# Optimization experiments

Measured on AMD Instinct MI355X. Metric: run time of the kernel, lower is better.

Reference implementation:

```python
import jax, jax.numpy as jnp
import numpy as np

N_ATOMS = 16384
N_EDGES = 524288
N_MOL = 256
A = 4            # num_pseudo_species
S = 4            # len(unique_numbers)
NMAX = 10        # radial basis size
NSPH = 9         # (l_max+1)^2 with l_max=2
Q = A * NMAX
NL = 3           # l_max+1
F = Q * Q * NL   # 4800 power-spectrum features
CUTOFF = 5.0
AVG_ATOMS = 64.0
SCALE = 1.0
H1, H2 = 512, 512


def _sph_l012(u):
    # real spherical harmonics l=0,1,2 on unit vectors u [E,3] -> [E,9]
    x, y, z = u[:, 0], u[:, 1], u[:, 2]
    c1 = 0.4886025119029199
    c2 = 1.0925484305920792
    return jnp.stack([
        jnp.full_like(x, 0.28209479177387814),
        c1 * y, c1 * z, c1 * x,
        c2 * x * y, c2 * y * z,
        0.31539156525252005 * (3.0 * z * z - 1.0),
        c2 * x * z,
        0.5462742152960396 * (x * x - y * y),
    ], axis=-1)


def _forward(positions, cells, edge_offsets, U, gamma, beta, W1, W2, W3, Wc,
             numbers, edge_indices, batch):
    send, recv = edge_indices[0], edge_indices[1]
    cell_e = cells[batch[send]]                                  # [E,3,3]
    rvec = positions[recv] - positions[send] + jnp.einsum('ek,ekl->el', edge_offsets, cell_e)
    r = jnp.sqrt(jnp.sum(rvec * rvec, axis=-1) + 1e-12)          # [E]
    rhat = rvec / r[:, None]
    fc = 0.5 * (jnp.cos(jnp.pi * r / CUTOFF) + 1.0) * (r < CUTOFF)
    mu = jnp.linspace(0.0, CUTOFF, NMAX)
    sig = CUTOFF / NMAX
    R = jnp.exp(-((r[:, None] - mu) ** 2) / (2.0 * sig * sig)) * fc[:, None]  # [E,NMAX]
    Y = _sph_l012(rhat)                                          # [E,9]
    RY = jnp.einsum('en,ek->enk', R, Y)                          # [E,NMAX,9]
    w = U[:, numbers[send]]                                      # [A,E] pseudo-species mix of neighbor species
    # spherical expansion per atom: c[i,a,n,lm]
    c = jnp.stack([jax.ops.segment_sum(w[a][:, None, None] * RY, recv, num_segments=N_ATOMS)
                   for a in range(A)], axis=1)                   # [N,A,NMAX,9]
    c = c.reshape(N_ATOMS, Q, NSPH)
    # power spectrum: contract over m within each l block, normalize by sqrt(2l+1)
    lblocks = [(0, 1, 1.0), (1, 4, 3.0), (4, 9, 5.0)]
    ps = jnp.stack([jnp.einsum('iqm,ipm->iqp', c[:, :, a:b], c[:, :, a:b]) / jnp.sqrt(nl)
                    for a, b, nl in lblocks], axis=-1).reshape(N_ATOMS, F)
    # layer norm
    mean = ps.mean(axis=-1, keepdims=True)
    var = ps.var(axis=-1, keepdims=True)
    x = (ps - mean) / jnp.sqrt(var + 1e-5) * gamma + beta

    def contract(x, W):
        # species-indexed contraction: per-species weight via combination matrix U
        Wsp = jnp.einsum('as,aio->sio', U, W)                    # [S,in,out]
        out = jnp.zeros((x.shape[0], W.shape[-1]), x.dtype)
        for s in range(S):                                       # small fixed species set
            out = out + jnp.where((numbers == s)[:, None], x @ Wsp[s], 0.0)
        return out

    x = jax.nn.silu(contract(x, W1))
    x = jax.nn.silu(contract(x, W2))
    x = contract(x, W3)                                          # [N,1]
    e = jax.ops.segment_sum(x, batch, num_segments=N_MOL)        # [M,1]
    e = e / jnp.sqrt(float(A)) / AVG_ATOMS
    comp = jax.ops.segment_sum(jax.nn.one_hot(numbers, S, dtype=x.dtype), batch, num_segments=N_MOL)
    return e * SCALE + comp @ Wc.T


def setup_inputs() -> dict:
    key = jax.random.key(0)
    ks = jax.random.split(key, 10)
    positions = jax.random.normal(ks[0], (N_ATOMS, 3), dtype=jnp.float32)
    cells = jnp.zeros((N_MOL, 3, 3), dtype=jnp.float32)
    numbers = jax.random.randint(ks[1], (N_ATOMS,), 0, S)
    edge_indices = jax.random.randint(ks[2], (2, N_EDGES), 0, N_ATOMS)
    edge_offsets = jnp.zeros((N_EDGES, 3), dtype=jnp.float32)
    batch = jnp.sort(jax.random.randint(ks[3], (N_ATOMS,), 0, N_MOL))
    U = jax.random.normal(ks[4], (A, S), dtype=jnp.float32) * 0.5
    gamma = jnp.ones((F,), dtype=jnp.float32)
    beta = jnp.zeros((F,), dtype=jnp.float32)
    W1 = jax.random.normal(ks[5], (A, F, H1), dtype=jnp.float32) / np.sqrt(F)
    W2 = jax.random.normal(ks[6], (A, H1, H2), dtype=jnp.float32) / np.sqrt(H1)
    W3 = jax.random.normal(ks[7], (A, H2, 1), dtype=jnp.float32) / np.sqrt(H2)
    Wc = jax.random.normal(ks[8], (1, S), dtype=jnp.float32) * 0.1
    return {"positions": positions, "cells": cells, "numbers": numbers,
            "edge_indices": edge_indices, "edge_offsets": edge_offsets, "batch": batch,
            "U": U, "gamma": gamma, "beta": beta, "W1": W1, "W2": W2, "W3": W3, "Wc": Wc}


def reference(positions, cells, numbers, edge_indices, edge_offsets, batch,
              U, gamma, beta, W1, W2, W3, Wc):
    return _forward(positions, cells, edge_offsets, U, gamma, beta, W1, W2, W3, Wc,
                    numbers, edge_indices, batch)
```

## Files before the change

kernel.cpp:

```cpp
#include <hip/hip_runtime.h>

#define NA   16384
#define NE   524288
#define NM   256
#define FF   4800
#define FR   2688
#define HH   512
#define NMX  10
#define NSPH 9

typedef __bf16 bf16x8 __attribute__((ext_vector_type(8)));
typedef float  f32x4  __attribute__((ext_vector_type(4)));
typedef unsigned short u16x8 __attribute__((ext_vector_type(8)));

__device__ inline unsigned short f2bf(float x){
  unsigned int u = __builtin_bit_cast(unsigned int, x);
  u += 0x7fffu + ((u >> 16) & 1u);
  return (unsigned short)(u >> 16);
}
__device__ inline float bf2f(unsigned short h){
  unsigned int u = ((unsigned int)h) << 16;
  return __builtin_bit_cast(float, u);
}
__device__ inline void atomic_add_f(float* p, float v){
  __hip_atomic_fetch_add(p, v, __ATOMIC_RELAXED, __HIP_MEMORY_SCOPE_AGENT);
}
__device__ inline void gload16(const void* g, void* l){
  __builtin_amdgcn_global_load_lds(
      (const __attribute__((address_space(1))) unsigned int*)g,
      (__attribute__((address_space(3))) unsigned int*)l, 16, 0, 0);
}
__device__ inline float silu(float x){ return x / (1.f + __expf(-x)); }

__device__ inline void decode_blk(int b, int& qb, int& pb){
  int q = 0, rem = b;
  while (rem >= 10 - q){ rem -= 10 - q; q++; }
  qb = q; pb = q + rem;
}

template<int CNT>
__device__ inline void ps_block(const float* __restrict__ cl, int qb, int pb, int off,
                                float nrm, bool diag, unsigned short* ob,
                                float& s1, float& s2){
  float cq[4][CNT], cp[4][CNT];
  #pragma unroll
  for (int i = 0; i < 4; i++)
    #pragma unroll
    for (int k = 0; k < CNT; k++){
      cq[i][k] = cl[(qb*4 + i)*9 + off + k];
      cp[i][k] = cl[(pb*4 + i)*9 + off + k];
    }
  #pragma unroll
  for (int qi = 0; qi < 4; qi++)
    #pragma unroll
    for (int pi = 0; pi < 4; pi++){
      float v = 0.f;
      #pragma unroll
      for (int k = 0; k < CNT; k++) v += cq[qi][k] * cp[pi][k];
      v *= nrm;
      float wgt = diag ? ((qi < pi) ? 2.f : ((qi == pi) ? 1.f : 0.f)) : 2.f;
      if (diag && qi > pi) v = 0.f;
      ob[qi*4 + pi] = f2bf(v);
      s1 += wgt * v;
      s2 += wgt * v * v;
    }
}

template<int CNT>
__device__ inline void ps_block_half(const float* __restrict__ cl, int qb, int pb, int off,
                                     float nrm, bool diag, int qh, unsigned short* ob,
                                     float& s1, float& s2){
  float cq[2][CNT], cp[4][CNT];
  #pragma unroll
  for (int i = 0; i < 2; i++)
    #pragma unroll
    for (int k = 0; k < CNT; k++)
      cq[i][k] = cl[(qb*4 + qh*2 + i)*9 + off + k];
  #pragma unroll
  for (int i = 0; i < 4; i++)
    #pragma unroll
    for (int k = 0; k < CNT; k++)
      cp[i][k] = cl[(pb*4 + i)*9 + off + k];
  #pragma unroll
  for (int qi = 0; qi < 2; qi++)
    #pragma unroll
    for (int pi = 0; pi < 4; pi++){
      int qg = qh*2 + qi;
      float v = 0.f;
      #pragma unroll
      for (int k = 0; k < CNT; k++) v += cq[qi][k] * cp[pi][k];
      v *= nrm;
      float wgt = diag ? ((qg < pi) ? 2.f : ((qg == pi) ? 1.f : 0.f)) : 2.f;
      if (diag && qg > pi) v = 0.f;
      ob[qi*4 + pi] = f2bf(v);
      s1 += wgt * v;
      s2 += wgt * v * v;
    }
}

__device__ inline int block_scan_excl(int v, int tid, int* lds){
  int lane = tid & 63, w = tid >> 6;
  int x = v;
  #pragma unroll
  for (int d = 1; d < 64; d <<= 1){
    int y = __shfl_up(x, d, 64);
    if (lane >= d) x += y;
  }
  if (lane == 63) lds[w] = x;
  __syncthreads();
  int wsum = 0;
  for (int i = 0; i < w; i++) wsum += lds[i];
  return wsum + x - v;
}

__global__ __launch_bounds__(256) void k_hist(const int* __restrict__ ei,
                                              const int* __restrict__ numbers,
                                              int* __restrict__ cnt64k){
  int e = blockIdx.x * 256 + threadIdx.x;
  if (e < NE){
    int key = ei[NE + e] * 4 + numbers[ei[e]];
    atomicAdd(&cnt64k[key], 1);
  }
}

__global__ __launch_bounds__(256) void k_scanA(const int* __restrict__ cnt64k,
                                               int* __restrict__ bsum){
  __shared__ int lds[4];
  int tid = threadIdx.x;
  int v = cnt64k[blockIdx.x * 256 + tid];
  int lane = tid & 63;
  #pragma unroll
  for (int m = 32; m; m >>= 1) v += __shfl_xor(v, m, 64);
  if (lane == 0) lds[tid >> 6] = v;
  __syncthreads();
  if (tid == 0) bsum[blockIdx.x] = lds[0] + lds[1] + lds[2] + lds[3];
}

__global__ __launch_bounds__(256) void k_scanB(const int* __restrict__ bsum,
                                               int* __restrict__ boff, int* __restrict__ starts){
  __shared__ int lds[4];
  int tid = threadIdx.x;
  int v = bsum[tid];
  int e = block_scan_excl(v, tid, lds);
  boff[tid] = e;
  if (tid == 0) starts[65536] = NE;
}

__global__ __launch_bounds__(256) void k_scanC(const int* __restrict__ cnt64k,
                                               const int* __restrict__ boff,
                                               int* __restrict__ starts, int* __restrict__ cursor){
  __shared__ int lds[4];
  int tid = threadIdx.x;
  int bin = blockIdx.x * 256 + tid;
  int v = cnt64k[bin];
  int e = block_scan_excl(v, tid, lds) + boff[blockIdx.x];
  starts[bin] = e;
  cursor[bin] = e;
}

__global__ __launch_bounds__(256) void k_sortperm(const int* __restrict__ ei,
                                                  const int* __restrict__ numbers,
                                                  int* __restrict__ cursor, int* __restrict__ perm){
  int e = blockIdx.x * 256 + threadIdx.x;
  if (e < NE){
    int key = ei[NE + e] * 4 + numbers[ei[e]];
    int p = atomicAdd(&cursor[key], 1);
    perm[p] = e;
  }
}

__global__ __launch_bounds__(256) void k_acount(const int* __restrict__ numbers,
                                                int* __restrict__ bhist){
  __shared__ int h[4];
  int tid = threadIdx.x;
  if (tid < 4) h[tid] = 0;
  __syncthreads();
  atomicAdd(&h[numbers[blockIdx.x * 256 + tid]], 1);
  __syncthreads();
  if (tid < 4) bhist[blockIdx.x * 4 + tid] = h[tid];
}

__global__ void k_aoffs(const int* __restrict__ bhist, int* __restrict__ boffs,
                        int* __restrict__ ints){
  if (threadIdx.x == 0){
    int* cnt = ints; int* offs = ints + 8;
    int tot[4] = {0,0,0,0};
    for (int b = 0; b < 64; b++)
      for (int s = 0; s < 4; s++) tot[s] += bhist[b*4 + s];
    int o = 0;
    for (int s = 0; s < 4; s++){ cnt[s] = tot[s]; offs[s] = o; o += tot[s]; }
    offs[4] = o;
    int run[4];
    for (int s = 0; s < 4; s++) run[s] = offs[s];
    for (int b = 0; b < 64; b++)
      for (int s = 0; s < 4; s++){ boffs[b*4 + s] = run[s]; run[s] += bhist[b*4 + s]; }
  }
}

__global__ __launch_bounds__(256) void k_aplace(const int* __restrict__ numbers,
                                                const int* __restrict__ boffs,
                                                int* __restrict__ list){
  __shared__ int ws[4][4];
  int tid = threadIdx.x, w = tid >> 6, lane = tid & 63;
  int i = blockIdx.x * 256 + tid;
  int sp = numbers[i];
  int rank = 0;
  #pragma unroll
  for (int s = 0; s < 4; s++){
    unsigned long long m = __ballot(sp == s);
    if (s == sp) rank = __popcll(m & (((unsigned long long)1 << lane) - 1));
    if (lane == 0) ws[w][s] = __popcll(m);
  }
  __syncthreads();
  int pre = 0;
  for (int w2 = 0; w2 < w; w2++) pre += ws[w2][sp];
  list[boffs[blockIdx.x * 4 + sp] + pre + rank] = i;
}

__global__ __launch_bounds__(384) void k_atom(
    const float* __restrict__ pos, const float* __restrict__ cells,
    const int* __restrict__ ei, const float* __restrict__ eoff,
    const int* __restrict__ batch, const int* __restrict__ startsK,
    const int* __restrict__ perm, const float* __restrict__ U,
    unsigned short* __restrict__ ps, float* __restrict__ stats)
{
  __shared__ float Rl[64][NMX];
  __shared__ float Yl[64][NSPH];
  __shared__ float csr[360];
  __shared__ float cl[360];
  __shared__ float red[16];
  __shared__ float ul[16];
  int atom = blockIdx.x;
  int tid = threadIdx.x;
  if (tid < 16) ul[tid] = U[tid];
  int e0 = startsK[atom * 4], e1 = startsK[atom * 4 + 4];
  float px = pos[atom*3+0], py = pos[atom*3+1], pz = pos[atom*3+2];
  int sp = tid / 90, n = (tid % 90) / 9, k = tid % 9;
  int aS = 0, aE = 0;
  if (tid < 360){ aS = startsK[atom * 4 + sp]; aE = startsK[atom * 4 + sp + 1]; }
  float acc = 0.f;
  for (int base = e0; base < e1; base += 64){
    int nch = min(64, e1 - base);
    if (tid < nch){
      int e = perm[base + tid];
      int snd = ei[e];
      const float* C = cells + (size_t)batch[snd] * 9;
      float o0 = eoff[e*3+0], o1 = eoff[e*3+1], o2 = eoff[e*3+2];
      float rx = px - pos[snd*3+0] + o0*C[0] + o1*C[3] + o2*C[6];
      float ry = py - pos[snd*3+1] + o0*C[1] + o1*C[4] + o2*C[7];
      float rz = pz - pos[snd*3+2] + o0*C[2] + o1*C[5] + o2*C[8];
      float r = sqrtf(rx*rx + ry*ry + rz*rz + 1e-12f);
      float inv = 1.f / r;
      float hx = rx*inv, hy = ry*inv, hz = rz*inv;
      float fc = (r < 5.f) ? (0.5f * (__cosf(r * 0.6283185307179586f) + 1.f)) : 0.f;
      #pragma unroll
      for (int nn = 0; nn < NMX; nn++){
        float d = r - (5.f/9.f) * (float)nn;
        Rl[tid][nn] = __expf(-2.f * d * d) * fc;
      }
      Yl[tid][0] = 0.28209479177387814f;
      Yl[tid][1] = 0.4886025119029199f * hy;
      Yl[tid][2] = 0.4886025119029199f * hz;
      Yl[tid][3] = 0.4886025119029199f * hx;
      Yl[tid][4] = 1.0925484305920792f * hx * hy;
      Yl[tid][5] = 1.0925484305920792f * hy * hz;
      Yl[tid][6] = 0.31539156525252005f * (3.f * hz * hz - 1.f);
      Yl[tid][7] = 1.0925484305920792f * hx * hz;
      Yl[tid][8] = 0.5462742152960396f * (hx * hx - hy * hy);
    }
    __syncthreads();
    if (tid < 360){
      int lo2 = max(aS, base), hi2 = min(aE, base + nch);
      for (int e = lo2; e < hi2; e++){
        int j = e - base;
        acc += Rl[j][n] * Yl[j][k];
      }
    }
    __syncthreads();
  }
  if (tid < 360) csr[tid] = acc;
  __syncthreads();
  if (tid < 360){
    int a = tid / 90, nk = tid % 90;
    cl[tid] = ul[a*4+0]*csr[nk] + ul[a*4+1]*csr[90+nk]
            + ul[a*4+2]*csr[180+nk] + ul[a*4+3]*csr[270+nk];
  }
  __syncthreads();
  float s1 = 0.f, s2 = 0.f;
  int w6 = tid >> 6, b = tid & 63;
  if (w6 <= 3 && b < 55){
    int l = (w6 < 2) ? 2 : 1;
    int qh = w6 & 1;
    int qb, pb;
    decode_blk(b, qb, pb);
    bool diag = (qb == pb);
    unsigned short ob[8];
    if (l == 2) ps_block_half<5>(cl, qb, pb, 4, 0.4472135954999579f, diag, qh, ob, s1, s2);
    else        ps_block_half<3>(cl, qb, pb, 1, 0.5773502691896258f, diag, qh, ob, s1, s2);
    unsigned short* dst = ps + (size_t)atom * FR + b * 48 + l * 16 + qh * 8;
    *reinterpret_cast<u16x8*>(dst) = *(const u16x8*)ob;
  } else if (w6 == 4 && b < 55){
    int qb, pb;
    decode_blk(b, qb, pb);
    bool diag = (qb == pb);
    unsigned short ob[16];
    ps_block<1>(cl, qb, pb, 0, 1.f, diag, ob, s1, s2);
    unsigned short* dst = ps + (size_t)atom * FR + b * 48;
    *reinterpret_cast<u16x8*>(dst)     = *(const u16x8*)&ob[0];
    *reinterpret_cast<u16x8*>(dst + 8) = *(const u16x8*)&ob[8];
  } else if (w6 == 5 && b < 6){
    unsigned short zb[8] = {0,0,0,0,0,0,0,0};
    *reinterpret_cast<u16x8*>(ps + (size_t)atom * FR + 2640 + b * 8) = *(const u16x8*)zb;
  }
  #pragma unroll
  for (int m = 32; m; m >>= 1){ s1 += __shfl_xor(s1, m, 64); s2 += __shfl_xor(s2, m, 64); }
  int w = tid >> 6, lane = tid & 63;
  if (lane == 0){ red[w] = s1; red[8 + w] = s2; }
  __syncthreads();
  if (tid == 0){
    float t1 = 0.f, t2 = 0.f;
    for (int i = 0; i < 6; i++){ t1 += red[i]; t2 += red[8 + i]; }
    float mean = t1 * (1.f / FF);
    float var = t2 * (1.f / FF) - mean * mean;
    var = fmaxf(var, 0.f);
    stats[2*atom]   = mean;
    stats[2*atom+1] = rsqrtf(var + 1e-5f);
  }
}

__global__ __launch_bounds__(256) void k_wg3(
    const float* __restrict__ W1, const float* __restrict__ U,
    const float* __restrict__ gamma, const float* __restrict__ beta,
    unsigned short* __restrict__ Wg, float* __restrict__ gW, float* __restrict__ bW)
{
  __shared__ unsigned short og[4][64][64];
  int n0 = blockIdx.x * 64, f0 = blockIdx.y * 64;
  int tid = threadIdx.x, ni = tid & 63;
  float u[4][4];
  #pragma unroll
  for (int a = 0; a < 4; a++)
    #pragma unroll
    for (int s = 0; s < 4; s++) u[a][s] = U[a*4 + s];
  float gs[4] = {0,0,0,0}, bs[4] = {0,0,0,0};
  for (int rep = 0; rep < 16; rep++){
    int fi = rep * 4 + (tid >> 6);
    int fp = f0 + fi;
    int b = fp / 48, r = fp % 48;
    int l = r >> 4, qi = (r >> 2) & 3, pi = r & 3;
    float tg[4] = {0,0,0,0}, tb[4] = {0,0,0,0};
    if (b < 55){
      int qb, pb;
      decode_blk(b, qb, pb);
      bool zero = (qb == pb) && (qi > pi);
      if (!zero){
        int q = qb*4 + qi, p = pb*4 + pi;
        int fa = (q * 40 + p) * 3 + l;
        float ga = gamma[fa], ba = beta[fa];
        float wm[4] = {0,0,0,0};
        #pragma unroll
        for (int a = 0; a < 4; a++){
          float wa = W1[(size_t)a * FF * 512 + (size_t)fa * 512 + n0 + ni];
          #pragma unroll
          for (int s = 0; s < 4; s++) wm[s] += u[a][s] * wa;
        }
        #pragma unroll
        for (int s = 0; s < 4; s++){ tg[s] = ga * wm[s]; tb[s] = ba * wm[s]; }
        if (p != q){
          int fb = (p * 40 + q) * 3 + l;
          float gb = gamma[fb], bb = beta[fb];
          float wn[4] = {0,0,0,0};
          #pragma unroll
          for (int a = 0; a < 4; a++){
            float wb = W1[(size_t)a * FF * 512 + (size_t)fb * 512 + n0 + ni];
            #pragma unroll
            for (int s = 0; s < 4; s++) wn[s] += u[a][s] * wb;
          }
          #pragma unroll
          for (int s = 0; s < 4; s++){ tg[s] += gb * wn[s]; tb[s] += bb * wn[s]; }
        }
      }
    }
    #pragma unroll
    for (int s = 0; s < 4; s++){
      og[s][fi][ni] = f2bf(tg[s]);
      gs[s] += tg[s];
      bs[s] += tb[s];
    }
  }
  #pragma unroll
  for (int s = 0; s < 4; s++){
    atomic_add_f(&gW[s * 512 + n0 + ni], gs[s]);
    atomic_add_f(&bW[s * 512 + n0 + ni], bs[s]);
  }
  __syncthreads();
  for (int it = 0; it < 8; it++){
    int idx = it * 256 + tid;
    int c = idx & 7;
    int rrow = idx >> 3;
    int s = rrow >> 6, nn = rrow & 63;
    unsigned short o[8];
    #pragma unroll
    for (int j = 0; j < 8; j++) o[j] = og[s][c*8 + j][nn];
    *reinterpret_cast<u16x8*>(&Wg[((size_t)s * 512 + n0 + nn) * FR + f0 + c * 8]) = *(const u16x8*)o;
  }
}

__global__ __launch_bounds__(256) void k_w2t(
    const float* __restrict__ W2, const float* __restrict__ U,
    unsigned short* __restrict__ W2t)
{
  __shared__ float t[64][65];
  int n0 = blockIdx.x * 64, k0 = blockIdx.y * 64, s = blockIdx.z;
  float u0 = U[s], u1 = U[4+s], u2 = U[8+s], u3 = U[12+s];
  int tid = threadIdx.x;
  #pragma unroll 4
  for (int rep = 0; rep < 16; rep++){
    int idx = rep * 256 + tid;
    int ki = idx >> 6, ni = idx & 63;
    size_t base = (size_t)(k0 + ki) * 512 + (n0 + ni);
    t[ki][ni] = u0*W2[base] + u1*W2[base + 512*512]
              + u2*W2[base + 2*512*512] + u3*W2[base + 3*512*512];
  }
  __syncthreads();
  #pragma unroll 4
  for (int rep = 0; rep < 16; rep++){
    int idx = rep * 256 + tid;
    int ni = idx >> 6, ki = idx & 63;
    W2t[((size_t)s * 512 + n0 + ni) * 512 + k0 + ki] = f2bf(t[ki][ni]);
  }
}

__global__ void k_w3(const float* __restrict__ W3, const float* __restrict__ U,
                     float* __restrict__ W3s)
{
  int idx = blockIdx.x * 256 + threadIdx.x;
  if (idx < 4 * 512){
    int s = idx >> 9, k = idx & 511;
    W3s[idx] = U[s]*W3[k] + U[4+s]*W3[512+k] + U[8+s]*W3[2*512+k] + U[12+s]*W3[3*512+k];
  }
}

template<int EPI, int NSPLIT>
__global__ __launch_bounds__(256) void k_gemm(
    const unsigned short* __restrict__ Ag, int lda, int K,
    const unsigned short* __restrict__ Btg,
    const int* __restrict__ list, const int* __restrict__ offs, const int* __restrict__ cnt,
    unsigned short* __restrict__ pout,
    const float* __restrict__ W3s, float* __restrict__ pacc)
{
  __shared__ alignas(16) char smem[32768];
  const int NV = 4 * NSPLIT;
  int b = blockIdx.x;
  int y = (b & 7) + 8 * (b / (8 * NV));
  int v = (b >> 3) % NV;
  int x = v & 3, kh = v >> 2;

  int s = 0, t = y;
  for (; s < 4; s++){
    int nts = (cnt[s] + 127) >> 7;
    if (t < nts) break;
    t -= nts;
  }
  if (s >= 4) return;
  int cntS = cnt[s], offS = offs[s];
  int rt = t, n0 = x * 128;
  int tid = threadIdx.x, w = tid >> 6, lane = tid & 63;
  int wr = w >> 1, wc = w & 1;

  const unsigned short* Bts = Btg + (size_t)s * 512 * K;
  const unsigned short* gA[4];
  const unsigned short* gB[4];
  char* lA[4];
  char* lB[4];
  #pragma unroll
  for (int it = 0; it < 4; it++){
    int g = it * 4 + w;
    int idx = g * 64 + lane;
    int row = idx >> 3, ch = idx & 7;
    int cg = ch ^ (row & 7);
    int gr = rt * 128 + row; gr = gr < cntS ? gr : cntS - 1;
    int atom = list[offS + gr];
    gA[it] = Ag + (size_t)atom * lda + cg * 8;
    lA[it] = smem + g * 1024;
    gB[it] = Bts + (size_t)(n0 + row) * K + cg * 8;
    lB[it] = smem + 16384 + g * 1024;
  }

  int hi = lane >> 4, lo = lane & 15;
  f32x4 acc[4][4];
  #pragma unroll
  for (int mi = 0; mi < 4; mi++)
    #pragma unroll
    for (int ni = 0; ni < 4; ni++)
      #pragma unroll
      for (int r = 0; r < 4; r++) acc[mi][ni][r] = 0.f;

  int abase[4], a7[4], bbase[4], b7[4];
  #pragma unroll
  for (int mi = 0; mi < 4; mi++){ int row = wr*64 + mi*16 + lo; abase[mi] = row*128; a7[mi] = row & 7; }
  #pragma unroll
  for (int ni = 0; ni < 4; ni++){ int row = wc*64 + ni*16 + lo; bbase[ni] = 16384 + row*128; b7[ni] = row & 7; }

  int nk = K / 64;
  int k0 = ((nk * kh) / NSPLIT) * 64;
  int k1 = ((nk * (kh + 1)) / NSPLIT) * 64;

  for (int kt = k0; kt < k1; kt += 64){
    #pragma unroll
    for (int it = 0; it < 4; it++) gload16(gA[it] + kt, lA[it]);
    #pragma unroll
    for (int it = 0; it < 4; it++) gload16(gB[it] + kt, lB[it]);
    __syncthreads();
    #pragma unroll
    for (int kk = 0; kk < 2; kk++){
      bf16x8 af[4], bfr[4];
      #pragma unroll
      for (int mi = 0; mi < 4; mi++)
        af[mi] = *(const bf16x8*)(smem + abase[mi] + (((kk*4 + hi) ^ a7[mi]) << 4));
      #pragma unroll
      for (int ni = 0; ni < 4; ni++)
        bfr[ni] = *(const bf16x8*)(smem + bbase[ni] + (((kk*4 + hi) ^ b7[ni]) << 4));
      #pragma unroll
      for (int mi = 0; mi < 4; mi++)
        #pragma unroll
        for (int ni = 0; ni < 4; ni++)
          acc[mi][ni] = __builtin_amdgcn_mfma_f32_16x16x32_bf16(af[mi], bfr[ni], acc[mi][ni], 0, 0, 0);
    }
    __syncthreads();
  }

  int gn[4];
  #pragma unroll
  for (int ni = 0; ni < 4; ni++) gn[ni] = n0 + wc*64 + ni*16 + lo;

  if (EPI == 0){
    #pragma unroll
    for (int mi = 0; mi < 4; mi++){
      #pragma unroll
      for (int j = 0; j < 4; j++){
        int gr = rt*128 + wr*64 + mi*16 + hi*4 + j;
        if (gr < cntS){
          int atom = list[offS + gr];
          #pragma unroll
          for (int ni = 0; ni < 4; ni++)
            pout[((size_t)kh * NA + atom) * 512 + gn[ni]] = f2bf(acc[mi][ni][j]);
        }
      }
    }
  } else {
    float w3v[4];
    #pragma unroll
    for (int ni = 0; ni < 4; ni++) w3v[ni] = W3s[s * 512 + gn[ni]];
    float* pslot = pacc + (size_t)(x * 2 + wc) * NA;
    #pragma unroll
    for (int mi = 0; mi < 4; mi++){
      #pragma unroll
      for (int j = 0; j < 4; j++){
        int gr = rt*128 + wr*64 + mi*16 + hi*4 + j;
        if (gr < cntS){
          int atom = list[offS + gr];
          float pdot = 0.f;
          #pragma unroll
          for (int ni = 0; ni < 4; ni++)
            pdot += silu(acc[mi][ni][j]) * w3v[ni];
          pdot += __shfl_xor(pdot, 1, 16);
          pdot += __shfl_xor(pdot, 2, 16);
          pdot += __shfl_xor(pdot, 4, 16);
          pdot += __shfl_xor(pdot, 8, 16);
          if (lo == 0) pslot[atom] = pdot;
        }
      }
    }
  }
}

__global__ __launch_bounds__(256) void k_epi(
    const unsigned short* __restrict__ pbuf, const float* __restrict__ stats,
    const float* __restrict__ gW, const float* __restrict__ bW,
    const int* __restrict__ numbers, unsigned short* __restrict__ h1)
{
  int w = threadIdx.x >> 6, lane = threadIdx.x & 63;
  int atom = blockIdx.x * 4 + w;
  int s = numbers[atom];
  float mean = stats[2*atom], rstd = stats[2*atom+1];
  int c0 = lane * 8;
  u16x8 a0 = *reinterpret_cast<const u16x8*>(pbuf + (size_t)atom * 512 + c0);
  u16x8 a1 = *reinterpret_cast<const u16x8*>(pbuf + (size_t)(NA + atom) * 512 + c0);
  u16x8 a2 = *reinterpret_cast<const u16x8*>(pbuf + (size_t)(2*NA + atom) * 512 + c0);
  u16x8 a3 = *reinterpret_cast<const u16x8*>(pbuf + (size_t)(3*NA + atom) * 512 + c0);
  unsigned short o[8];
  #pragma unroll
  for (int j = 0; j < 8; j++){
    int c = c0 + j;
    float acc = (bf2f(a0[j]) + bf2f(a1[j])) + (bf2f(a2[j]) + bf2f(a3[j]));
    float vv = rstd * acc + bW[s*512 + c] - mean * rstd * gW[s*512 + c];
    o[j] = f2bf(silu(vv));
  }
  *reinterpret_cast<u16x8*>(h1 + (size_t)atom * 512 + c0) = *(const u16x8*)o;
}

__global__ __launch_bounds__(256) void k_final2(
    const float* __restrict__ pacc, const int* __restrict__ numbers,
    const int* __restrict__ batch, const float* __restrict__ Wc,
    float* __restrict__ molOut)
{
  int atom = blockIdx.x * 256 + threadIdx.x;
  int lane = threadIdx.x & 63;
  float sum = 0.f;
  #pragma unroll
  for (int p = 0; p < 8; p++) sum += pacc[(size_t)p * NA + atom];
  float val = sum * (1.f / 128.f) + Wc[numbers[atom]];
  int mol = batch[atom];
  int m0 = __shfl(mol, 0, 64);
  int m63 = __shfl(mol, 63, 64);
  if (m0 == m63){
    #pragma unroll
    for (int m = 32; m; m >>= 1) val += __shfl_xor(val, m, 64);
    if (lane == 0) atomic_add_f(&molOut[mol], val);
  } else {
    atomic_add_f(&molOut[mol], val);
  }
}

extern "C" void kernel_launch(void* const* d_in, const int* in_sizes, int n_in,
                              void* d_out, int out_size, void* d_ws, size_t ws_size,
                              hipStream_t stream)
{
  const float* pos     = (const float*)d_in[0];
  const float* cells   = (const float*)d_in[1];
  const int*   numbers = (const int*)d_in[2];
  const int*   ei      = (const int*)d_in[3];
  const float* eoff    = (const float*)d_in[4];
  const int*   batch   = (const int*)d_in[5];
  const float* U       = (const float*)d_in[6];
  const float* gamma   = (const float*)d_in[7];
  const float* beta    = (const float*)d_in[8];
  const float* W1      = (const float*)d_in[9];
  const float* W2      = (const float*)d_in[10];
  const float* W3      = (const float*)d_in[11];
  const float* Wc      = (const float*)d_in[12];
  float* out = (float*)d_out;

  char* ws = (char*)d_ws;
  size_t off = 0;
  auto alloc = [&](size_t bytes) -> void* {
    void* p = ws + off;
    off += (bytes + 255) & ~(size_t)255;
    return p;
  };
  unsigned short* ps   = (unsigned short*)alloc((size_t)NA * FR * 2);
  unsigned short* pbuf = (unsigned short*)alloc((size_t)4 * NA * 512 * 2);
  float* stats         = (float*)alloc((size_t)NA * 2 * 4);
  unsigned short* Wg1  = (unsigned short*)alloc((size_t)4 * 512 * FR * 2);
  unsigned short* W2t  = (unsigned short*)alloc((size_t)4 * 512 * 512 * 2);
  float* W3s           = (float*)alloc(4 * 512 * 4);
  unsigned short* h1   = (unsigned short*)alloc((size_t)NA * 512 * 2);
  float* pacc          = (float*)alloc((size_t)8 * NA * 4);
  int* list            = (int*)alloc(NA * 4);
  int* perm            = (int*)alloc((size_t)NE * 4);
  int* startsK         = (int*)alloc((65536 + 1) * 4);
  int* cnt64k          = (int*)alloc(65536 * 4);
  float* gW            = (float*)alloc(4 * 512 * 4);
  float* bW            = (float*)alloc(4 * 512 * 4);
  int* cursor64k       = (int*)alloc(65536 * 4);
  int* bsum            = (int*)alloc(256 * 4);
  int* boff            = (int*)alloc(256 * 4);
  int* bhist           = (int*)alloc(64 * 4 * 4);
  int* boffs           = (int*)alloc(64 * 4 * 4);
  int* ints            = (int*)alloc(64);
  int* cnt = ints; int* offs = ints + 8;

  hipMemsetAsync(cnt64k, 0, 65536 * 4 + 2 * 4 * 512 * 4, stream);
  hipMemsetAsync(out, 0, (size_t)out_size * 4, stream);

  k_hist<<<NE / 256, 256, 0, stream>>>(ei, numbers, cnt64k);
  k_scanA<<<256, 256, 0, stream>>>(cnt64k, bsum);
  k_scanB<<<1, 256, 0, stream>>>(bsum, boff, startsK);
  k_scanC<<<256, 256, 0, stream>>>(cnt64k, boff, startsK, cursor64k);
  k_sortperm<<<NE / 256, 256, 0, stream>>>(ei, numbers, cursor64k, perm);

  k_acount<<<NA / 256, 256, 0, stream>>>(numbers, bhist);
  k_aoffs<<<1, 64, 0, stream>>>(bhist, boffs, ints);
  k_aplace<<<NA / 256, 256, 0, stream>>>(numbers, boffs, list);

  k_atom<<<NA, 384, 0, stream>>>(pos, cells, ei, eoff, batch, startsK, perm, U, ps, stats);

  k_wg3<<<dim3(8, 42), 256, 0, stream>>>(W1, U, gamma, beta, Wg1, gW, bW);
  k_w2t<<<dim3(8, 8, 4), 256, 0, stream>>>(W2, U, W2t);
  k_w3<<<8, 256, 0, stream>>>(W3, U, W3s);

  k_gemm<0, 4><<<2176, 256, 0, stream>>>(ps, FR, FR, Wg1, list, offs, cnt,
                                         pbuf, nullptr, nullptr);
  k_epi<<<NA / 4, 256, 0, stream>>>(pbuf, stats, gW, bW, numbers, h1);

  k_gemm<2, 1><<<544, 256, 0, stream>>>(h1, 512, 512, W2t, list, offs, cnt,
                                        nullptr, W3s, pacc);
  k_final2<<<NA / 256, 256, 0, stream>>>(pacc, numbers, batch, Wc, out);
}
```

Baseline: 319.0 us.

## Compute layer-norm stats from Gram identities and fuse setup kernels

Measured after the change: 314.6 us. About the same (-1.4%).

```diff
diff --git a/kernel.cpp b/kernel.cpp
--- a/kernel.cpp
+++ b/kernel.cpp
@@ -13,10 +13,11 @@
 typedef float  f32x4  __attribute__((ext_vector_type(4)));
 typedef unsigned short u16x8 __attribute__((ext_vector_type(8)));
 
+__constant__ int g_ka[22] = {0, 1,1,1,2,2,3, 4,4,4,4,4, 5,5,5,5, 6,6,6, 7,7, 8};
+__constant__ int g_kb[22] = {0, 1,2,3,2,3,3, 4,5,6,7,8, 5,6,7,8, 6,7,8, 7,8, 8};
+
 __device__ inline unsigned short f2bf(float x){
-  unsigned int u = __builtin_bit_cast(unsigned int, x);
-  u += 0x7fffu + ((u >> 16) & 1u);
-  return (unsigned short)(u >> 16);
+  return __builtin_bit_cast(unsigned short, (__bf16)x);
 }
 __device__ inline float bf2f(unsigned short h){
   unsigned int u = ((unsigned int)h) << 16;
@@ -40,8 +41,7 @@
 
 template<int CNT>
 __device__ inline void ps_block(const float* __restrict__ cl, int qb, int pb, int off,
-                                float nrm, bool diag, unsigned short* ob,
-                                float& s1, float& s2){
+                                float nrm, bool diag, unsigned short* ob){
   float cq[4][CNT], cp[4][CNT];
   #pragma unroll
   for (int i = 0; i < 4; i++)
@@ -58,18 +58,14 @@
       #pragma unroll
       for (int k = 0; k < CNT; k++) v += cq[qi][k] * cp[pi][k];
       v *= nrm;
-      float wgt = diag ? ((qi < pi) ? 2.f : ((qi == pi) ? 1.f : 0.f)) : 2.f;
       if (diag && qi > pi) v = 0.f;
       ob[qi*4 + pi] = f2bf(v);
-      s1 += wgt * v;
-      s2 += wgt * v * v;
     }
 }
 
 template<int CNT>
 __device__ inline void ps_block_half(const float* __restrict__ cl, int qb, int pb, int off,
-                                     float nrm, bool diag, int qh, unsigned short* ob,
-                                     float& s1, float& s2){
+                                     float nrm, bool diag, int qh, unsigned short* ob){
   float cq[2][CNT], cp[4][CNT];
   #pragma unroll
   for (int i = 0; i < 2; i++)
@@ -90,11 +86,8 @@
       #pragma unroll
       for (int k = 0; k < CNT; k++) v += cq[qi][k] * cp[pi][k];
       v *= nrm;
-      float wgt = diag ? ((qg < pi) ? 2.f : ((qg == pi) ? 1.f : 0.f)) : 2.f;
       if (diag && qg > pi) v = 0.f;
       ob[qi*4 + pi] = f2bf(v);
-      s1 += wgt * v;
-      s2 += wgt * v * v;
     }
 }
 
@@ -115,11 +108,20 @@
 
 __global__ __launch_bounds__(256) void k_hist(const int* __restrict__ ei,
                                               const int* __restrict__ numbers,
-                                              int* __restrict__ cnt64k){
-  int e = blockIdx.x * 256 + threadIdx.x;
-  if (e < NE){
+                                              int* __restrict__ cnt64k,
+                                              int* __restrict__ bhist){
+  __shared__ int h[4];
+  int blk = blockIdx.x, tid = threadIdx.x;
+  if (blk < 2048){
+    int e = blk * 256 + tid;
     int key = ei[NE + e] * 4 + numbers[ei[e]];
     atomicAdd(&cnt64k[key], 1);
+  } else {
+    if (tid < 4) h[tid] = 0;
+    __syncthreads();
+    atomicAdd(&h[numbers[(blk - 2048) * 256 + tid]], 1);
+    __syncthreads();
+    if (tid < 4) bhist[(blk - 2048) * 4 + tid] = h[tid];
   }
 }
 
@@ -137,52 +139,16 @@
 }
 
 __global__ __launch_bounds__(256) void k_scanB(const int* __restrict__ bsum,
-                                               int* __restrict__ boff, int* __restrict__ starts){
+                                               int* __restrict__ boff, int* __restrict__ starts,
+                                               const int* __restrict__ bhist,
+                                               int* __restrict__ boffs, int* __restrict__ ints){
   __shared__ int lds[4];
   int tid = threadIdx.x;
   int v = bsum[tid];
   int e = block_scan_excl(v, tid, lds);
   boff[tid] = e;
-  if (tid == 0) starts[65536] = NE;
-}
-
-__global__ __launch_bounds__(256) void k_scanC(const int* __restrict__ cnt64k,
-                                               const int* __restrict__ boff,
-                                               int* __restrict__ starts, int* __restrict__ cursor){
-  __shared__ int lds[4];
-  int tid = threadIdx.x;
-  int bin = blockIdx.x * 256 + tid;
-  int v = cnt64k[bin];
-  int e = block_scan_excl(v, tid, lds) + boff[blockIdx.x];
-  starts[bin] = e;
-  cursor[bin] = e;
-}
-
-__global__ __launch_bounds__(256) void k_sortperm(const int* __restrict__ ei,
-                                                  const int* __restrict__ numbers,
-                                                  int* __restrict__ cursor, int* __restrict__ perm){
-  int e = blockIdx.x * 256 + threadIdx.x;
-  if (e < NE){
-    int key = ei[NE + e] * 4 + numbers[ei[e]];
-    int p = atomicAdd(&cursor[key], 1);
-    perm[p] = e;
-  }
-}
-
-__global__ __launch_bounds__(256) void k_acount(const int* __restrict__ numbers,
-                                                int* __restrict__ bhist){
-  __shared__ int h[4];
-  int tid = threadIdx.x;
-  if (tid < 4) h[tid] = 0;
-  __syncthreads();
-  atomicAdd(&h[numbers[blockIdx.x * 256 + tid]], 1);
-  __syncthreads();
-  if (tid < 4) bhist[blockIdx.x * 4 + tid] = h[tid];
-}
-
-__global__ void k_aoffs(const int* __restrict__ bhist, int* __restrict__ boffs,
-                        int* __restrict__ ints){
-  if (threadIdx.x == 0){
+  if (tid == 0){
+    starts[65536] = NE;
     int* cnt = ints; int* offs = ints + 8;
     int tot[4] = {0,0,0,0};
     for (int b = 0; b < 64; b++)
@@ -197,6 +163,29 @@
   }
 }
 
+__global__ __launch_bounds__(256) void k_scanC(const int* __restrict__ cnt64k,
+                                               const int* __restrict__ boff,
+                                               int* __restrict__ starts, int* __restrict__ cursor){
+  __shared__ int lds[4];
+  int tid = threadIdx.x;
+  int bin = blockIdx.x * 256 + tid;
+  int v = cnt64k[bin];
+  int e = block_scan_excl(v, tid, lds) + boff[blockIdx.x];
+  starts[bin] = e;
+  cursor[bin] = e;
+}
+
+__global__ __launch_bounds__(256) void k_sortperm(const int* __restrict__ ei,
+                                                  const int* __restrict__ numbers,
+                                                  int* __restrict__ cursor, int* __restrict__ perm){
+  int e = blockIdx.x * 256 + threadIdx.x;
+  if (e < NE){
+    int key = ei[NE + e] * 4 + numbers[ei[e]];
+    int p = atomicAdd(&cursor[key], 1);
+    perm[p] = e;
+  }
+}
+
 __global__ __launch_bounds__(256) void k_aplace(const int* __restrict__ numbers,
                                                 const int* __restrict__ boffs,
                                                 int* __restrict__ list){
@@ -228,7 +217,6 @@
   __shared__ float Yl[64][NSPH];
   __shared__ float csr[360];
   __shared__ float cl[360];
-  __shared__ float red[16];
   __shared__ float ul[16];
   int atom = blockIdx.x;
   int tid = threadIdx.x;
@@ -286,7 +274,6 @@
             + ul[a*4+2]*csr[180+nk] + ul[a*4+3]*csr[270+nk];
   }
   __syncthreads();
-  float s1 = 0.f, s2 = 0.f;
   int w6 = tid >> 6, b = tid & 63;
   if (w6 <= 3 && b < 55){
     int l = (w6 < 2) ? 2 : 1;
@@ -295,8 +282,8 @@
     decode_blk(b, qb, pb);
     bool diag = (qb == pb);
     unsigned short ob[8];
-    if (l == 2) ps_block_half<5>(cl, qb, pb, 4, 0.4472135954999579f, diag, qh, ob, s1, s2);
-    else        ps_block_half<3>(cl, qb, pb, 1, 0.5773502691896258f, diag, qh, ob, s1, s2);
+    if (l == 2) ps_block_half<5>(cl, qb, pb, 4, 0.4472135954999579f, diag, qh, ob);
+    else        ps_block_half<3>(cl, qb, pb, 1, 0.5773502691896258f, diag, qh, ob);
     unsigned short* dst = ps + (size_t)atom * FR + b * 48 + l * 16 + qh * 8;
     *reinterpret_cast<u16x8*>(dst) = *(const u16x8*)ob;
   } else if (w6 == 4 && b < 55){
@@ -304,27 +291,40 @@
     decode_blk(b, qb, pb);
     bool diag = (qb == pb);
     unsigned short ob[16];
-    ps_block<1>(cl, qb, pb, 0, 1.f, diag, ob, s1, s2);
+    ps_block<1>(cl, qb, pb, 0, 1.f, diag, ob);
     unsigned short* dst = ps + (size_t)atom * FR + b * 48;
     *reinterpret_cast<u16x8*>(dst)     = *(const u16x8*)&ob[0];
     *reinterpret_cast<u16x8*>(dst + 8) = *(const u16x8*)&ob[8];
-  } else if (w6 == 5 && b < 6){
-    unsigned short zb[8] = {0,0,0,0,0,0,0,0};
-    *reinterpret_cast<u16x8*>(ps + (size_t)atom * FR + 2640 + b * 8) = *(const u16x8*)zb;
-  }
-  #pragma unroll
-  for (int m = 32; m; m >>= 1){ s1 += __shfl_xor(s1, m, 64); s2 += __shfl_xor(s2, m, 64); }
-  int w = tid >> 6, lane = tid & 63;
-  if (lane == 0){ red[w] = s1; red[8 + w] = s2; }
-  __syncthreads();
-  if (tid == 0){
-    float t1 = 0.f, t2 = 0.f;
-    for (int i = 0; i < 6; i++){ t1 += red[i]; t2 += red[8 + i]; }
-    float mean = t1 * (1.f / FF);
-    float var = t2 * (1.f / FF) - mean * mean;
-    var = fmaxf(var, 0.f);
-    stats[2*atom]   = mean;
-    stats[2*atom+1] = rsqrtf(var + 1e-5f);
+  } else if (w6 == 5){
+    if (b < 6){
+      unsigned short zb[8] = {0,0,0,0,0,0,0,0};
+      *reinterpret_cast<u16x8*>(ps + (size_t)atom * FR + 2640 + b * 8) = *(const u16x8*)zb;
+    }
+    float c1 = 0.f, c2 = 0.f;
+    if (b >= 8 && b < 17){
+      int kk = b - 8;
+      float S = 0.f;
+      for (int q = 0; q < 40; q++) S += cl[q*9 + kk];
+      float nrm = (kk == 0) ? 1.f : ((kk < 4) ? 0.5773502691896258f : 0.4472135954999579f);
+      c1 = nrm * S * S;
+    } else if (b >= 24 && b < 46){
+      int j = b - 24;
+      int ka = g_ka[j], kb = g_kb[j];
+      float G = 0.f;
+      for (int q = 0; q < 40; q++) G += cl[q*9 + ka] * cl[q*9 + kb];
+      float n2 = (ka == 0) ? 1.f : ((ka < 4) ? (1.f/3.f) : 0.2f);
+      float mul = (ka == kb) ? 1.f : 2.f;
+      c2 = n2 * mul * G * G;
+    }
+    #pragma unroll
+    for (int m = 32; m; m >>= 1){ c1 += __shfl_xor(c1, m, 64); c2 += __shfl_xor(c2, m, 64); }
+    if (b == 0){
+      float mean = c1 * (1.f / FF);
+      float var = c2 * (1.f / FF) - mean * mean;
+      var = fmaxf(var, 0.f);
+      stats[2*atom]   = mean;
+      stats[2*atom+1] = rsqrtf(var + 1e-5f);
+    }
   }
 }
 
@@ -673,14 +673,11 @@
   hipMemsetAsync(cnt64k, 0, 65536 * 4 + 2 * 4 * 512 * 4, stream);
   hipMemsetAsync(out, 0, (size_t)out_size * 4, stream);
 
-  k_hist<<<NE / 256, 256, 0, stream>>>(ei, numbers, cnt64k);
+  k_hist<<<2048 + 64, 256, 0, stream>>>(ei, numbers, cnt64k, bhist);
   k_scanA<<<256, 256, 0, stream>>>(cnt64k, bsum);
-  k_scanB<<<1, 256, 0, stream>>>(bsum, boff, startsK);
+  k_scanB<<<1, 256, 0, stream>>>(bsum, boff, startsK, bhist, boffs, ints);
   k_scanC<<<256, 256, 0, stream>>>(cnt64k, boff, startsK, cursor64k);
   k_sortperm<<<NE / 256, 256, 0, stream>>>(ei, numbers, cursor64k, perm);
-
-  k_acount<<<NA / 256, 256, 0, stream>>>(numbers, bhist);
-  k_aoffs<<<1, 64, 0, stream>>>(bhist, boffs, ints);
   k_aplace<<<NA / 256, 256, 0, stream>>>(numbers, boffs, list);
 
   k_atom<<<NA, 384, 0, stream>>>(pos, cells, ei, eoff, batch, startsK, perm, U, ps, stats);
```
